# Optimization experiments

Hardware: AMD Instinct MI355X
Metric: run time of the kernel (lower is better)

Reference implementation:

```python
import jax, jax.numpy as jnp
import numpy as np
import math

C = 256
NUM_CLASSES = 80
NUM_CONVS = 4
GROUPS = 32
LEVEL_SHAPES = [(100, 152), (50, 76), (25, 38), (13, 19), (7, 10)]
BATCH = 2


def conv2d(x, w, b):
    # x: [N,C,H,W], w: [O,I,3,3] -> SAME padding, stride 1
    y = jax.lax.conv_general_dilated(x, w, window_strides=(1, 1), padding='SAME',
                                     dimension_numbers=('NCHW', 'OIHW', 'NCHW'))
    return y + b[None, :, None, None]


def group_norm(x, w, b, groups=GROUPS, eps=1e-5):
    N, Ch, H, W = x.shape
    xg = x.reshape(N, groups, Ch // groups, H, W)
    mu = jnp.mean(xg, axis=(2, 3, 4), keepdims=True)
    var = jnp.var(xg, axis=(2, 3, 4), keepdims=True)
    xg = (xg - mu) * jax.lax.rsqrt(var + eps)
    x = xg.reshape(N, Ch, H, W)
    return x * w[None, :, None, None] + b[None, :, None, None]


def tower(x, cw, cb, gw, gb):
    for i in range(NUM_CONVS):
        x = jax.nn.relu(group_norm(conv2d(x, cw[i], cb[i]), gw[i], gb[i]))
    return x


def flatten_head(y, c):
    # [N, A*c, H, W] -> [N, H*W*A, c]  (matches view/permute/reshape in torch)
    N, AC, H, W = y.shape
    A = AC // c
    return y.reshape(N, A, c, H, W).transpose(0, 3, 4, 1, 2).reshape(N, H * W * A, c)


def setup_inputs() -> dict:
    key = jax.random.key(0)
    ks = iter(jax.random.split(key, 64))
    inp = {}
    for i, (h, w) in enumerate(LEVEL_SHAPES):
        inp[f"feat{i}"] = jax.random.normal(next(ks), (BATCH, C, h, w), jnp.float32)
    def cw(shape):  # conv weights init std=0.01 as in torch module
        return jax.random.normal(next(ks), shape, jnp.float32) * 0.01
    inp["cls_conv_w"] = cw((NUM_CONVS, C, C, 3, 3))
    inp["cls_conv_b"] = jnp.zeros((NUM_CONVS, C), jnp.float32)
    inp["cls_gn_w"] = jnp.ones((NUM_CONVS, C), jnp.float32)
    inp["cls_gn_b"] = jnp.zeros((NUM_CONVS, C), jnp.float32)
    inp["cls_out_w"] = cw((NUM_CLASSES, C, 3, 3))
    inp["cls_out_b"] = jnp.full((NUM_CLASSES,), -math.log(99.0), jnp.float32)  # prior prob 0.01
    inp["reg_conv_w"] = cw((NUM_CONVS, C, C, 3, 3))
    inp["reg_conv_b"] = jnp.zeros((NUM_CONVS, C), jnp.float32)
    inp["reg_gn_w"] = jnp.ones((NUM_CONVS, C), jnp.float32)
    inp["reg_gn_b"] = jnp.zeros((NUM_CONVS, C), jnp.float32)
    for name, oc in [("bbox", 4), ("ctr", 1), ("dim", 3), ("ori", 1), ("kp", 16), ("depth", 1)]:
        inp[f"{name}_w"] = cw((oc, C, 3, 3))
        inp[f"{name}_b"] = jnp.zeros((oc,), jnp.float32)
    return inp


def reference(feat0, feat1, feat2, feat3, feat4,
              cls_conv_w, cls_conv_b, cls_gn_w, cls_gn_b, cls_out_w, cls_out_b,
              reg_conv_w, reg_conv_b, reg_gn_w, reg_gn_b,
              bbox_w, bbox_b, ctr_w, ctr_b, dim_w, dim_b,
              ori_w, ori_b, kp_w, kp_b, depth_w, depth_b):
    feats = [feat0, feat1, feat2, feat3, feat4]
    cls_all, bbox_all, ctr_all, dim_all, ori_all, kp_all, depth_all = ([] for _ in range(7))
    for f in feats:
        cf = tower(f, cls_conv_w, cls_conv_b, cls_gn_w, cls_gn_b)
        cls_all.append(flatten_head(conv2d(cf, cls_out_w, cls_out_b), NUM_CLASSES))
        rf = tower(f, reg_conv_w, reg_conv_b, reg_gn_w, reg_gn_b)
        bbox_all.append(flatten_head(jax.nn.relu(conv2d(rf, bbox_w, bbox_b)), 4))
        ctr_all.append(flatten_head(conv2d(rf, ctr_w, ctr_b), 1))
        dim_all.append(flatten_head(conv2d(rf, dim_w, dim_b), 3))
        ori_all.append(flatten_head(conv2d(rf, ori_w, ori_b), 1))
        kp_all.append(flatten_head(conv2d(rf, kp_w, kp_b), 16))
        depth_all.append(flatten_head(conv2d(rf, depth_w, depth_b), 1))
    cat = lambda xs: jnp.concatenate(xs, axis=1)
    return (cat(cls_all), cat(bbox_all), cat(ctr_all), cat(dim_all),
            cat(ori_all), cat(kp_all), cat(depth_all))
```

## Files before the change

kernel.cpp:

```cpp
#include <hip/hip_runtime.h>
#include <stdint.h>

typedef unsigned short ushort_t;
typedef __bf16 bf16x8 __attribute__((ext_vector_type(8)));
typedef float f32x4 __attribute__((ext_vector_type(4)));

#define TOTAL_HW 20267
#define PTOT 21267

__constant__ int d_RB[26] = {3242720,3242720,3242720,3242720, 3404856, 3445390,3445390,3445390,
                             3566992, 3607526,3607526,3607526,3607526,3607526,3607526,3607526,3607526,
                             3607526,3607526,3607526,3607526,3607526,3607526,3607526,3607526, 4256070};
__constant__ int d_RM[26] = {4,4,4,4, 1, 3,3,3, 1, 16,16,16,16,16,16,16,16,16,16,16,16,16,16,16,16, 1};
__constant__ int d_RC[26] = {0,1,2,3, 0, 0,1,2, 0, 0,1,2,3,4,5,6,7,8,9,10,11,12,13,14,15, 0};

__constant__ int F_TC[6]   = {0,238,298,314,318,320};
__constant__ int F_TL[5]   = {119,30,8,2,1};
__constant__ int F_W[5]    = {152,76,38,19,10};
__constant__ int F_HW[5]   = {15200,3800,950,247,70};
__constant__ int F_PB[5]   = {0,15708,19764,20844,21159};
__constant__ int F_LOFF[5] = {0,15200,19000,19950,20197};
__constant__ int F_PC[6]   = {0,508,764,894,962,1000};
__constant__ int F_H[5]    = {100,50,25,13,7};

__device__ __forceinline__ ushort_t f2bf(float f) {
    union { float f; uint32_t i; } x; x.f = f;
    uint32_t r = x.i + 0x7fffu + ((x.i >> 16) & 1u);
    return (ushort_t)(r >> 16);
}
__device__ __forceinline__ float bf2f(ushort_t u) {
    union { uint32_t i; float f; } x; x.i = ((uint32_t)u) << 16; return x.f;
}
__device__ __forceinline__ void gld16(const ushort_t* g, ushort_t* lds) {
    __builtin_amdgcn_global_load_lds((const __attribute__((address_space(1))) void*)g,
                                     (__attribute__((address_space(3))) void*)lds, 16, 0, 0);
}

__global__ __launch_bounds__(256) void wtrans_towerall_k(const float* __restrict__ cw,
                                                         const float* __restrict__ rw,
                                                         ushort_t* __restrict__ dst)
{
    int id = blockIdx.x * 256 + threadIdx.x;
    int g = id >> 16;
    int oc = (id >> 8) & 255, ic = id & 255;
    const float* base = (g >= 4) ? rw : cw;
    int L = g & 3;
    const float* s = base + (size_t)L * 589824 + (size_t)(oc * 256 + ic) * 9;
    ushort_t* d = dst + (size_t)g * 589824 + oc * 256 + ic;
    #pragma unroll
    for (int t = 0; t < 9; t++) d[t * 65536] = f2bf(s[t]);
}
__global__ __launch_bounds__(256) void wtrans_cls_k(const float* __restrict__ src,
                                                    ushort_t* __restrict__ dst)
{
    int id = blockIdx.x * 256 + threadIdx.x;
    int oc = id >> 8, ic = id & 255;
    ushort_t* d = dst + oc * 256 + ic;
    if (oc < 80) {
        const float* s = src + (size_t)(oc * 256 + ic) * 9;
        #pragma unroll
        for (int t = 0; t < 9; t++) d[t * 32768] = f2bf(s[t]);
    } else {
        #pragma unroll
        for (int t = 0; t < 9; t++) d[t * 32768] = 0;
    }
}
__global__ __launch_bounds__(256) void wtrans_reg_k(
    const float* bbox_w, const float* ctr_w, const float* dim_w,
    const float* ori_w,  const float* kp_w,  const float* depth_w,
    const float* bbox_b, const float* ctr_b, const float* dim_b,
    const float* ori_b,  const float* kp_b,  const float* depth_b,
    ushort_t* __restrict__ dst, float* __restrict__ RegBias)
{
    int id = blockIdx.x * 256 + threadIdx.x;
    int oc = id >> 8, ic = id & 255;
    ushort_t* d = dst + oc * 256 + ic;
    if (oc < 26) {
        const float* s; int c;
        if (oc < 4)       { s = bbox_w;  c = oc; }
        else if (oc < 5)  { s = ctr_w;   c = 0; }
        else if (oc < 8)  { s = dim_w;   c = oc - 5; }
        else if (oc < 9)  { s = ori_w;   c = 0; }
        else if (oc < 25) { s = kp_w;    c = oc - 9; }
        else              { s = depth_w; c = 0; }
        const float* sp = s + (size_t)(c * 256 + ic) * 9;
        #pragma unroll
        for (int t = 0; t < 9; t++) d[t * 32768] = f2bf(sp[t]);
    } else {
        #pragma unroll
        for (int t = 0; t < 9; t++) d[t * 32768] = 0;
    }
    if (id < 26) {
        const float* b; int c;
        if (id < 4)       { b = bbox_b;  c = id; }
        else if (id < 5)  { b = ctr_b;   c = 0; }
        else if (id < 8)  { b = dim_b;   c = id - 5; }
        else if (id < 9)  { b = ori_b;   c = 0; }
        else if (id < 25) { b = kp_b;    c = id - 9; }
        else              { b = depth_b; c = 0; }
        RegBias[id] = b[c];
    }
}

__global__ __launch_bounds__(256) void pad_k(ushort_t* b0, ushort_t* b1, ushort_t* b2, ushort_t* b3)
{
    int u = blockIdx.x * 256 + threadIdx.x;
    if (u >= 256000) return;
    int chunk = u & 31; u >>= 5;
    int buf = u & 3; u >>= 2;
    int n = (u >= 1000) ? 1 : 0; int pidx = u - n * 1000;
    int l = 0;
    #pragma unroll
    for (int i = 1; i < 5; i++) if (pidx >= F_PC[i]) l = i;
    int q = pidx - F_PC[l];
    int W = F_W[l], H = F_H[l], Wp = W + 2;
    int py, px;
    if (q < Wp) { py = 0; px = q; }
    else if (q < 2 * Wp) { py = H + 1; px = q - Wp; }
    else { int q2 = q - 2 * Wp; py = 1 + (q2 >> 1); px = (q2 & 1) ? (Wp - 1) : 0; }
    ushort_t* base = b0;
    if (buf == 1) base = b1; else if (buf == 2) base = b2; else if (buf == 3) base = b3;
    *(uint4*)(base + ((size_t)n * PTOT + F_PB[l] + py * Wp + px) * 256 + chunk * 8) = uint4{0u,0u,0u,0u};
}

__global__ __launch_bounds__(256) void packF_k(
    const float* f0, const float* f1, const float* f2,
    const float* f3, const float* f4, ushort_t* __restrict__ S)
{
    __shared__ ushort_t tile[64][65];
    const int PCUM[6] = {0, 1904, 2384, 2504, 2536, 2552};
    const int PT[5]   = {238, 60, 15, 4, 2};
    int bid = blockIdx.x;
    int l = 0;
    #pragma unroll
    for (int i = 1; i < 5; i++) if (bid >= PCUM[i]) l = i;
    int r = bid - PCUM[l];
    int per_n = PT[l] * 4;
    int n = (r >= per_n) ? 1 : 0; r -= n * per_n;
    int pb = r >> 2, cb = r & 3;
    const float* fs = f0;
    if (l == 1) fs = f1; else if (l == 2) fs = f2; else if (l == 3) fs = f3; else if (l == 4) fs = f4;
    int HW = F_HW[l], W = F_W[l], Wp = W + 2;
    int p0 = pb * 64, c0 = cb * 64;
    int t = threadIdx.x;
    #pragma unroll
    for (int i = 0; i < 16; i++) {
        int idx = i * 256 + t; int cl = idx >> 6, pl = idx & 63;
        int p = p0 + pl; ushort_t v = 0;
        if (p < HW) v = f2bf(fs[(size_t)(n * 256 + c0 + cl) * HW + p]);
        tile[cl][pl] = v;
    }
    __syncthreads();
    ushort_t* ob = S + ((size_t)n * PTOT + F_PB[l]) * 256;
    #pragma unroll
    for (int i = 0; i < 16; i++) {
        int idx = i * 256 + t; int pl = idx >> 6, cl = idx & 63;
        int p = p0 + pl;
        if (p < HW) {
            int y = p / W, x = p - y * W;
            ob[((y + 1) * Wp + (x + 1)) * 256 + c0 + cl] = tile[cl][pl];
        }
    }
}

__global__ __launch_bounds__(512, 4) void convT_k(
    const ushort_t* __restrict__ srcC, const ushort_t* __restrict__ srcR,
    ushort_t* __restrict__ dstC, ushort_t* __restrict__ dstR,
    const ushort_t* __restrict__ wtAll,
    const float* __restrict__ biasC, const float* __restrict__ biasR,
    float* __restrict__ stats, int L)
{
    __shared__ __align__(16) ushort_t As[2][8192];
    __shared__ __align__(16) ushort_t Bs[2][8192];

    int gid = blockIdx.x;
    int xcd = gid & 7, idx = gid >> 3;
    int bid = xcd * 40 + (idx >> 2);
    int oc0 = (idx & 1) * 128;
    int tw = (idx >> 1) & 1;

    const ushort_t* src = tw ? srcR : srcC;
    ushort_t* dst = tw ? dstR : dstC;
    const ushort_t* wt = wtAll + (size_t)(tw * 4 + L) * 589824;
    const float* bias = (tw ? biasR : biasC) + L * 256;

    int l = 0;
    #pragma unroll
    for (int i = 1; i < 5; i++) if (bid >= F_TC[i]) l = i;
    int r = bid - F_TC[l];
    int tl = F_TL[l];
    int n = (r >= tl) ? 1 : 0; int tile = r - n * tl;
    int W = F_W[l], HW = F_HW[l], Wp = W + 2;
    int px0 = tile * 128;
    const ushort_t* sbase = src + ((size_t)n * PTOT + F_PB[l]) * 256;
    ushort_t* obase = dst + ((size_t)n * PTOT + F_PB[l]) * 256;

    int tid = threadIdx.x, wv = tid >> 6, ln = tid & 63;
    int wr = wv >> 2, wc = wv & 3;

    int aoff, boff;
    {
        int rloc = wv * 16 + (ln >> 2);
        int p = px0 + rloc; if (p > HW - 1) p = HW - 1;
        int y = p / W, x = p - y * W;
        int c = ((ln & 3) - (rloc >> 1)) & 3;
        aoff = ((y + 1) * Wp + (x + 1)) * 256 + c * 8;
        boff = (oc0 + rloc) * 256 + c * 8;
    }

    auto stage = [&](int it, int b) {
        int tp = it >> 2, q = it & 3;
        int ky = tp / 3, kx = tp - ky * 3;
        int tapo = ((ky - 1) * Wp + (kx - 1)) * 256 + (q << 6);
        const ushort_t* wtap = wt + tp * 65536 + (q << 6);
        gld16(sbase + aoff + tapo,      &As[b][wv * 512]);
        gld16(sbase + aoff + tapo + 32, &As[b][4096 + wv * 512]);
        gld16(wtap + boff,      &Bs[b][wv * 512]);
        gld16(wtap + boff + 32, &Bs[b][4096 + wv * 512]);
    };

    f32x4 acc[4][2];
    #pragma unroll
    for (int mi = 0; mi < 4; mi++)
        #pragma unroll
        for (int ni = 0; ni < 2; ni++) acc[mi][ni] = f32x4{0.f, 0.f, 0.f, 0.f};

    stage(0, 0);

    #pragma unroll 2
    for (int it = 0; it < 36; ++it) {
        asm volatile("s_waitcnt vmcnt(0) lgkmcnt(0)\n\ts_barrier" ::: "memory");
        if (it + 1 < 36) stage(it + 1, (it + 1) & 1);
        int b = it & 1;
        #pragma unroll
        for (int kh = 0; kh < 2; kh++) {
            bf16x8 af[4], bg[2];
            #pragma unroll
            for (int mi = 0; mi < 4; mi++) {
                int rA = wr * 64 + mi * 16 + (ln & 15);
                int ch = ((ln >> 4) + (rA >> 1)) & 3;
                af[mi] = *(const bf16x8*)&As[b][kh * 4096 + rA * 32 + ch * 8];
            }
            #pragma unroll
            for (int ni = 0; ni < 2; ni++) {
                int rB = wc * 32 + ni * 16 + (ln & 15);
                int ch = ((ln >> 4) + (rB >> 1)) & 3;
                bg[ni] = *(const bf16x8*)&Bs[b][kh * 4096 + rB * 32 + ch * 8];
            }
            __builtin_amdgcn_s_setprio(1);
            #pragma unroll
            for (int mi = 0; mi < 4; mi++)
                #pragma unroll
                for (int ni = 0; ni < 2; ni++)
                    acc[mi][ni] = __builtin_amdgcn_mfma_f32_16x16x32_bf16(af[mi], bg[ni], acc[mi][ni], 0, 0, 0);
            __builtin_amdgcn_s_setprio(0);
        }
    }

    #pragma unroll
    for (int ni = 0; ni < 2; ni++) {
        int oc = oc0 + wc * 32 + ni * 16 + (ln & 15);
        float bv = bias[oc];
        float s = 0.f, q = 0.f;
        #pragma unroll
        for (int mi = 0; mi < 4; mi++) {
            int pb = px0 + wr * 64 + mi * 16 + ((ln >> 4) << 2);
            if (pb < HW) {
                int y = pb / W, x = pb - y * W;
                #pragma unroll
                for (int rr2 = 0; rr2 < 4; rr2++) {
                    int p = pb + rr2;
                    if (p < HW) {
                        float v = acc[mi][ni][rr2] + bv;
                        obase[((y + 1) * Wp + (x + 1)) * 256 + oc] = f2bf(v);
                        s += v; q += v * v;
                    }
                    x++; if (x == W) { x = 0; y++; }
                }
            }
        }
        s += __shfl_xor(s, 16, 64); q += __shfl_xor(q, 16, 64);
        s += __shfl_xor(s, 32, 64); q += __shfl_xor(q, 32, 64);
        s += __shfl_xor(s, 1, 64);  q += __shfl_xor(q, 1, 64);
        s += __shfl_xor(s, 2, 64);  q += __shfl_xor(q, 2, 64);
        s += __shfl_xor(s, 4, 64);  q += __shfl_xor(q, 4, 64);
        if (ln == 0 || ln == 8) {
            int g = (oc0 + wc * 32 + ni * 16 + (ln & 8)) >> 3;
            float* st = stats + (size_t)((tw * 4 + L) * 5 + l) * 128 + (n * 32 + g) * 2;
            atomicAdd(st, s); atomicAdd(st + 1, q);
        }
    }
}

__global__ __launch_bounds__(512, 4) void convH_k(
    const ushort_t* __restrict__ srcC, const ushort_t* __restrict__ srcR,
    const ushort_t* __restrict__ wtC, const ushort_t* __restrict__ wtR,
    const float* __restrict__ biasC, const float* __restrict__ biasR,
    float* __restrict__ outF)
{
    __shared__ __align__(16) ushort_t As[2][8192];
    __shared__ __align__(16) ushort_t Bs[2][8192];

    int gid = blockIdx.x;
    int xcd = gid & 7, idx = gid >> 3;
    int bid = xcd * 40 + (idx >> 1);
    int mode = idx & 1;

    const ushort_t* src = mode ? srcR : srcC;
    const ushort_t* wt  = mode ? wtR  : wtC;
    const float* bias   = mode ? biasR : biasC;

    int l = 0;
    #pragma unroll
    for (int i = 1; i < 5; i++) if (bid >= F_TC[i]) l = i;
    int r = bid - F_TC[l];
    int tl = F_TL[l];
    int n = (r >= tl) ? 1 : 0; int tile = r - n * tl;
    int W = F_W[l], HW = F_HW[l], Wp = W + 2;
    int px0 = tile * 128;
    const ushort_t* sbase = src + ((size_t)n * PTOT + F_PB[l]) * 256;

    int tid = threadIdx.x, wv = tid >> 6, ln = tid & 63;
    int wr = wv >> 2, wc = wv & 3;

    int aoff, boff;
    {
        int rloc = wv * 16 + (ln >> 2);
        int p = px0 + rloc; if (p > HW - 1) p = HW - 1;
        int y = p / W, x = p - y * W;
        int c = ((ln & 3) - (rloc >> 1)) & 3;
        aoff = ((y + 1) * Wp + (x + 1)) * 256 + c * 8;
        boff = rloc * 256 + c * 8;
    }

    auto stage = [&](int it, int b) {
        int tp = it >> 2, q = it & 3;
        int ky = tp / 3, kx = tp - ky * 3;
        int tapo = ((ky - 1) * Wp + (kx - 1)) * 256 + (q << 6);
        const ushort_t* wtap = wt + tp * 32768 + (q << 6);
        gld16(sbase + aoff + tapo,      &As[b][wv * 512]);
        gld16(sbase + aoff + tapo + 32, &As[b][4096 + wv * 512]);
        gld16(wtap + boff,      &Bs[b][wv * 512]);
        gld16(wtap + boff + 32, &Bs[b][4096 + wv * 512]);
    };

    f32x4 acc[4][2];
    #pragma unroll
    for (int mi = 0; mi < 4; mi++)
        #pragma unroll
        for (int ni = 0; ni < 2; ni++) acc[mi][ni] = f32x4{0.f, 0.f, 0.f, 0.f};

    stage(0, 0);

    #pragma unroll 2
    for (int it = 0; it < 36; ++it) {
        asm volatile("s_waitcnt vmcnt(0) lgkmcnt(0)\n\ts_barrier" ::: "memory");
        if (it + 1 < 36) stage(it + 1, (it + 1) & 1);
        int b = it & 1;
        #pragma unroll
        for (int kh = 0; kh < 2; kh++) {
            bf16x8 af[4], bg[2];
            #pragma unroll
            for (int mi = 0; mi < 4; mi++) {
                int rA = wr * 64 + mi * 16 + (ln & 15);
                int ch = ((ln >> 4) + (rA >> 1)) & 3;
                af[mi] = *(const bf16x8*)&As[b][kh * 4096 + rA * 32 + ch * 8];
            }
            #pragma unroll
            for (int ni = 0; ni < 2; ni++) {
                int rB = wc * 32 + ni * 16 + (ln & 15);
                int ch = ((ln >> 4) + (rB >> 1)) & 3;
                bg[ni] = *(const bf16x8*)&Bs[b][kh * 4096 + rB * 32 + ch * 8];
            }
            __builtin_amdgcn_s_setprio(1);
            #pragma unroll
            for (int mi = 0; mi < 4; mi++)
                #pragma unroll
                for (int ni = 0; ni < 2; ni++)
                    acc[mi][ni] = __builtin_amdgcn_mfma_f32_16x16x32_bf16(af[mi], bg[ni], acc[mi][ni], 0, 0, 0);
            __builtin_amdgcn_s_setprio(0);
        }
    }

    #pragma unroll
    for (int ni = 0; ni < 2; ni++) {
        int oc = wc * 32 + ni * 16 + (ln & 15);
        bool valid = mode ? (oc < 26) : (oc < 80);
        if (valid) {
            float bv = bias[oc];
            int rb = 0, rm = 80, rc = oc; bool rl = false;
            if (mode) { rb = d_RB[oc]; rm = d_RM[oc]; rc = d_RC[oc]; rl = (oc < 4); }
            #pragma unroll
            for (int mi = 0; mi < 4; mi++) {
                int pb = px0 + wr * 64 + mi * 16 + ((ln >> 4) << 2);
                #pragma unroll
                for (int rr2 = 0; rr2 < 4; rr2++) {
                    int p = pb + rr2;
                    if (p < HW) {
                        float v = acc[mi][ni][rr2] + bv;
                        if (rl) v = fmaxf(v, 0.f);
                        int pg = n * TOTAL_HW + F_LOFF[l] + p;
                        outF[rb + (size_t)pg * rm + rc] = v;
                    }
                }
            }
        }
    }
}

__global__ __launch_bounds__(256) void normF_k(
    ushort_t* __restrict__ bufC, ushort_t* __restrict__ bufR,
    const float* __restrict__ stats,
    const float* __restrict__ gwC, const float* __restrict__ gwR,
    const float* __restrict__ gbC, const float* __restrict__ gbR, int L)
{
    int u = blockIdx.x * 256 + threadIdx.x;
    if (u >= 2594176) return;
    int tw = (u >= 1297088) ? 1 : 0; u -= tw * 1297088;
    int n = (u >= 648544) ? 1 : 0; u -= n * 648544;
    int cp = u >> 5, g = u & 31;
    int l = 0;
    #pragma unroll
    for (int i = 1; i < 5; i++) if (cp >= F_LOFF[i]) l = i;
    int p = cp - F_LOFF[l];
    int W = F_W[l], HW = F_HW[l];
    int y = p / W, x = p - y * W;
    const float* st = stats + (size_t)((tw * 4 + L) * 5 + l) * 128 + (n * 32 + g) * 2;
    float cnt = 8.0f * (float)HW;
    float mean = st[0] / cnt;
    float var = st[1] / cnt - mean * mean;
    float inv = rsqrtf(fmaxf(var, 0.f) + 1e-5f);
    const float* gw = (tw ? gwR : gwC) + L * 256 + g * 8;
    const float* gb = (tw ? gbR : gbC) + L * 256 + g * 8;
    ushort_t* buf = tw ? bufR : bufC;
    ushort_t* ptr = buf + (((size_t)n * PTOT + F_PB[l]) + (y + 1) * (W + 2) + (x + 1)) * 256 + g * 8;
    uint4 din = *(const uint4*)ptr;
    uint4 dout;
    const ushort_t* xi = (const ushort_t*)&din;
    ushort_t* oi = (ushort_t*)&dout;
    #pragma unroll
    for (int i = 0; i < 8; i++) {
        float v = (bf2f(xi[i]) - mean) * inv * gw[i] + gb[i];
        oi[i] = f2bf(fmaxf(v, 0.f));
    }
    *(uint4*)ptr = dout;
}


extern "C" void kernel_launch(void* const* d_in, const int* in_sizes, int n_in,
                              void* d_out, int out_size, void* d_ws, size_t ws_size,
                              hipStream_t stream) {
    const float* feats[5] = {(const float*)d_in[0], (const float*)d_in[1],
                             (const float*)d_in[2], (const float*)d_in[3],
                             (const float*)d_in[4]};
    const float* cls_conv_w = (const float*)d_in[5];
    const float* cls_conv_b = (const float*)d_in[6];
    const float* cls_gn_w   = (const float*)d_in[7];
    const float* cls_gn_b   = (const float*)d_in[8];
    const float* cls_out_w  = (const float*)d_in[9];
    const float* cls_out_b  = (const float*)d_in[10];
    const float* reg_conv_w = (const float*)d_in[11];
    const float* reg_conv_b = (const float*)d_in[12];
    const float* reg_gn_w   = (const float*)d_in[13];
    const float* reg_gn_b   = (const float*)d_in[14];

    char* wsb = (char*)d_ws;
    float* Stats     = (float*)wsb;
    float* RegBias   = (float*)(wsb + 20480);
    ushort_t* TowerWtAll = (ushort_t*)(wsb + 20608);
    ushort_t* WtCls  = (ushort_t*)(wsb + 9457792);
    ushort_t* WtReg  = (ushort_t*)(wsb + 10047616);
    ushort_t* S  = (ushort_t*)(wsb + 10637440);
    ushort_t* Ac = (ushort_t*)(wsb + 32414848);
    ushort_t* Ar = (ushort_t*)(wsb + 54192256);
    ushort_t* Br = (ushort_t*)(wsb + 75969664);
    float* outf  = (float*)d_out;

    hipMemsetAsync(d_ws, 0, 20608, stream);
    pad_k<<<1000, 256, 0, stream>>>(S, Ac, Ar, Br);

    wtrans_towerall_k<<<2048, 256, 0, stream>>>(cls_conv_w, reg_conv_w, TowerWtAll);
    wtrans_cls_k<<<128, 256, 0, stream>>>(cls_out_w, WtCls);
    wtrans_reg_k<<<128, 256, 0, stream>>>(
        (const float*)d_in[15], (const float*)d_in[17], (const float*)d_in[19],
        (const float*)d_in[21], (const float*)d_in[23], (const float*)d_in[25],
        (const float*)d_in[16], (const float*)d_in[18], (const float*)d_in[20],
        (const float*)d_in[22], (const float*)d_in[24], (const float*)d_in[26],
        WtReg, RegBias);

    packF_k<<<2552, 256, 0, stream>>>(feats[0], feats[1], feats[2], feats[3], feats[4], S);

    ushort_t* sc[4] = {S,  Ac, S,  Ac};
    ushort_t* dc[4] = {Ac, S,  Ac, S };
    ushort_t* sr[4] = {S,  Ar, Br, Ar};
    ushort_t* dr[4] = {Ar, Br, Ar, Br};
    for (int L = 0; L < 4; L++) {
        convT_k<<<1280, 512, 0, stream>>>(
            sc[L], sr[L], dc[L], dr[L], TowerWtAll, cls_conv_b, reg_conv_b, Stats, L);
        normF_k<<<10134, 256, 0, stream>>>(
            dc[L], dr[L], Stats, cls_gn_w, reg_gn_w, cls_gn_b, reg_gn_b, L);
    }
    convH_k<<<640, 512, 0, stream>>>(S, Br, WtCls, WtReg, cls_out_b, RegBias, outf);
}
```

Baseline: 789.9 us.

## Split K across wave halves with 64x64 warp tiles and LDS reduction

Both conv kernels change the wave layout from 2x4 waves each doing both K-halves of a 128x128 tile to a 2x2 spatial grid with two K-split groups. Each wave now computes a 64x64 sub-tile over one K-half, doubling MFMA work per LDS fragment load and cutting LDS read traffic per MFMA. The partial sums are then exchanged through shared memory and reduced, with each wave of a pair finishing half of the output columns. This doubles the accumulator registers and adds an epilogue LDS round trip plus two barriers, which may hurt occupancy under the 512x4 launch bounds.

```diff
diff --git a/kernel.cpp b/kernel.cpp
--- a/kernel.cpp
+++ b/kernel.cpp
@@ -170,8 +170,7 @@
     const float* __restrict__ biasC, const float* __restrict__ biasR,
     float* __restrict__ stats, int L)
 {
-    __shared__ __align__(16) ushort_t As[2][8192];
-    __shared__ __align__(16) ushort_t Bs[2][8192];
+    __shared__ __align__(16) ushort_t SH[32768];
 
     int gid = blockIdx.x;
     int xcd = gid & 7, idx = gid >> 3;
@@ -196,7 +195,7 @@
     ushort_t* obase = dst + ((size_t)n * PTOT + F_PB[l]) * 256;
 
     int tid = threadIdx.x, wv = tid >> 6, ln = tid & 63;
-    int wr = wv >> 2, wc = wv & 3;
+    int wr = (wv >> 1) & 1, wc = wv & 1, kh = wv >> 2;
 
     int aoff, boff;
     {
@@ -213,17 +212,17 @@
         int ky = tp / 3, kx = tp - ky * 3;
         int tapo = ((ky - 1) * Wp + (kx - 1)) * 256 + (q << 6);
         const ushort_t* wtap = wt + tp * 65536 + (q << 6);
-        gld16(sbase + aoff + tapo,      &As[b][wv * 512]);
-        gld16(sbase + aoff + tapo + 32, &As[b][4096 + wv * 512]);
-        gld16(wtap + boff,      &Bs[b][wv * 512]);
-        gld16(wtap + boff + 32, &Bs[b][4096 + wv * 512]);
+        gld16(sbase + aoff + tapo,      &SH[b * 8192 + wv * 512]);
+        gld16(sbase + aoff + tapo + 32, &SH[b * 8192 + 4096 + wv * 512]);
+        gld16(wtap + boff,      &SH[16384 + b * 8192 + wv * 512]);
+        gld16(wtap + boff + 32, &SH[16384 + b * 8192 + 4096 + wv * 512]);
     };
 
-    f32x4 acc[4][2];
+    f32x4 acc[4][4];
     #pragma unroll
     for (int mi = 0; mi < 4; mi++)
         #pragma unroll
-        for (int ni = 0; ni < 2; ni++) acc[mi][ni] = f32x4{0.f, 0.f, 0.f, 0.f};
+        for (int ni = 0; ni < 4; ni++) acc[mi][ni] = f32x4{0.f, 0.f, 0.f, 0.f};
 
     stage(0, 0);
 
@@ -232,34 +231,49 @@
         asm volatile("s_waitcnt vmcnt(0) lgkmcnt(0)\n\ts_barrier" ::: "memory");
         if (it + 1 < 36) stage(it + 1, (it + 1) & 1);
         int b = it & 1;
-        #pragma unroll
-        for (int kh = 0; kh < 2; kh++) {
-            bf16x8 af[4], bg[2];
+        bf16x8 af[4], bg[4];
+        #pragma unroll
+        for (int mi = 0; mi < 4; mi++) {
+            int rA = wr * 64 + mi * 16 + (ln & 15);
+            int ch = ((ln >> 4) + (rA >> 1)) & 3;
+            af[mi] = *(const bf16x8*)&SH[b * 8192 + kh * 4096 + rA * 32 + ch * 8];
+        }
+        #pragma unroll
+        for (int ni = 0; ni < 4; ni++) {
+            int rB = wc * 64 + ni * 16 + (ln & 15);
+            int ch = ((ln >> 4) + (rB >> 1)) & 3;
+            bg[ni] = *(const bf16x8*)&SH[16384 + b * 8192 + kh * 4096 + rB * 32 + ch * 8];
+        }
+        __builtin_amdgcn_s_setprio(1);
+        #pragma unroll
+        for (int mi = 0; mi < 4; mi++)
             #pragma unroll
-            for (int mi = 0; mi < 4; mi++) {
-                int rA = wr * 64 + mi * 16 + (ln & 15);
-                int ch = ((ln >> 4) + (rA >> 1)) & 3;
-                af[mi] = *(const bf16x8*)&As[b][kh * 4096 + rA * 32 + ch * 8];
-            }
-            #pragma unroll
-            for (int ni = 0; ni < 2; ni++) {
-                int rB = wc * 32 + ni * 16 + (ln & 15);
-                int ch = ((ln >> 4) + (rB >> 1)) & 3;
-                bg[ni] = *(const bf16x8*)&Bs[b][kh * 4096 + rB * 32 + ch * 8];
-            }
-            __builtin_amdgcn_s_setprio(1);
-            #pragma unroll
-            for (int mi = 0; mi < 4; mi++)
-                #pragma unroll
-                for (int ni = 0; ni < 2; ni++)
-                    acc[mi][ni] = __builtin_amdgcn_mfma_f32_16x16x32_bf16(af[mi], bg[ni], acc[mi][ni], 0, 0, 0);
-            __builtin_amdgcn_s_setprio(0);
-        }
-    }
-
-    #pragma unroll
-    for (int ni = 0; ni < 2; ni++) {
-        int oc = oc0 + wc * 32 + ni * 16 + (ln & 15);
+            for (int ni = 0; ni < 4; ni++)
+                acc[mi][ni] = __builtin_amdgcn_mfma_f32_16x16x32_bf16(af[mi], bg[ni], acc[mi][ni], 0, 0, 0);
+        __builtin_amdgcn_s_setprio(0);
+    }
+
+    __syncthreads();
+    f32x4* F4 = (f32x4*)SH;
+    int prt = wv ^ 4;
+    int wbase = kh ? 0 : 2;
+    int rbase = kh ? 2 : 0;
+    #pragma unroll
+    for (int mi = 0; mi < 4; mi++)
+        #pragma unroll
+        for (int h = 0; h < 2; h++)
+            F4[wv * 512 + ln * 8 + ((mi * 2 + h) ^ (ln & 7))] = acc[mi][wbase + h];
+    __syncthreads();
+    #pragma unroll
+    for (int mi = 0; mi < 4; mi++)
+        #pragma unroll
+        for (int h = 0; h < 2; h++)
+            acc[mi][rbase + h] += F4[prt * 512 + ln * 8 + ((mi * 2 + h) ^ (ln & 7))];
+
+    #pragma unroll
+    for (int h = 0; h < 2; h++) {
+        int ni = rbase + h;
+        int oc = oc0 + wc * 64 + ni * 16 + (ln & 15);
         float bv = bias[oc];
         float s = 0.f, q = 0.f;
         #pragma unroll
@@ -285,7 +299,7 @@
         s += __shfl_xor(s, 2, 64);  q += __shfl_xor(q, 2, 64);
         s += __shfl_xor(s, 4, 64);  q += __shfl_xor(q, 4, 64);
         if (ln == 0 || ln == 8) {
-            int g = (oc0 + wc * 32 + ni * 16 + (ln & 8)) >> 3;
+            int g = (oc0 + wc * 64 + ni * 16 + (ln & 8)) >> 3;
             float* st = stats + (size_t)((tw * 4 + L) * 5 + l) * 128 + (n * 32 + g) * 2;
             atomicAdd(st, s); atomicAdd(st + 1, q);
         }
@@ -298,8 +312,7 @@
     const float* __restrict__ biasC, const float* __restrict__ biasR,
     float* __restrict__ outF)
 {
-    __shared__ __align__(16) ushort_t As[2][8192];
-    __shared__ __align__(16) ushort_t Bs[2][8192];
+    __shared__ __align__(16) ushort_t SH[32768];
 
     int gid = blockIdx.x;
     int xcd = gid & 7, idx = gid >> 3;
@@ -321,7 +334,7 @@
     const ushort_t* sbase = src + ((size_t)n * PTOT + F_PB[l]) * 256;
 
     int tid = threadIdx.x, wv = tid >> 6, ln = tid & 63;
-    int wr = wv >> 2, wc = wv & 3;
+    int wr = (wv >> 1) & 1, wc = wv & 1, kh = wv >> 2;
 
     int aoff, boff;
     {
@@ -338,17 +351,17 @@
         int ky = tp / 3, kx = tp - ky * 3;
         int tapo = ((ky - 1) * Wp + (kx - 1)) * 256 + (q << 6);
         const ushort_t* wtap = wt + tp * 32768 + (q << 6);
-        gld16(sbase + aoff + tapo,      &As[b][wv * 512]);
-        gld16(sbase + aoff + tapo + 32, &As[b][4096 + wv * 512]);
-        gld16(wtap + boff,      &Bs[b][wv * 512]);
-        gld16(wtap + boff + 32, &Bs[b][4096 + wv * 512]);
+        gld16(sbase + aoff + tapo,      &SH[b * 8192 + wv * 512]);
+        gld16(sbase + aoff + tapo + 32, &SH[b * 8192 + 4096 + wv * 512]);
+        gld16(wtap + boff,      &SH[16384 + b * 8192 + wv * 512]);
+        gld16(wtap + boff + 32, &SH[16384 + b * 8192 + 4096 + wv * 512]);
     };
 
-    f32x4 acc[4][2];
+    f32x4 acc[4][4];
     #pragma unroll
     for (int mi = 0; mi < 4; mi++)
         #pragma unroll
-        for (int ni = 0; ni < 2; ni++) acc[mi][ni] = f32x4{0.f, 0.f, 0.f, 0.f};
+        for (int ni = 0; ni < 4; ni++) acc[mi][ni] = f32x4{0.f, 0.f, 0.f, 0.f};
 
     stage(0, 0);
 
@@ -357,34 +370,49 @@
         asm volatile("s_waitcnt vmcnt(0) lgkmcnt(0)\n\ts_barrier" ::: "memory");
         if (it + 1 < 36) stage(it + 1, (it + 1) & 1);
         int b = it & 1;
-        #pragma unroll
-        for (int kh = 0; kh < 2; kh++) {
-            bf16x8 af[4], bg[2];
+        bf16x8 af[4], bg[4];
+        #pragma unroll
+        for (int mi = 0; mi < 4; mi++) {
+            int rA = wr * 64 + mi * 16 + (ln & 15);
+            int ch = ((ln >> 4) + (rA >> 1)) & 3;
+            af[mi] = *(const bf16x8*)&SH[b * 8192 + kh * 4096 + rA * 32 + ch * 8];
+        }
+        #pragma unroll
+        for (int ni = 0; ni < 4; ni++) {
+            int rB = wc * 64 + ni * 16 + (ln & 15);
+            int ch = ((ln >> 4) + (rB >> 1)) & 3;
+            bg[ni] = *(const bf16x8*)&SH[16384 + b * 8192 + kh * 4096 + rB * 32 + ch * 8];
+        }
+        __builtin_amdgcn_s_setprio(1);
+        #pragma unroll
+        for (int mi = 0; mi < 4; mi++)
             #pragma unroll
-            for (int mi = 0; mi < 4; mi++) {
-                int rA = wr * 64 + mi * 16 + (ln & 15);
-                int ch = ((ln >> 4) + (rA >> 1)) & 3;
-                af[mi] = *(const bf16x8*)&As[b][kh * 4096 + rA * 32 + ch * 8];
-            }
-            #pragma unroll
-            for (int ni = 0; ni < 2; ni++) {
-                int rB = wc * 32 + ni * 16 + (ln & 15);
-                int ch = ((ln >> 4) + (rB >> 1)) & 3;
-                bg[ni] = *(const bf16x8*)&Bs[b][kh * 4096 + rB * 32 + ch * 8];
-            }
-            __builtin_amdgcn_s_setprio(1);
-            #pragma unroll
-            for (int mi = 0; mi < 4; mi++)
-                #pragma unroll
-                for (int ni = 0; ni < 2; ni++)
-                    acc[mi][ni] = __builtin_amdgcn_mfma_f32_16x16x32_bf16(af[mi], bg[ni], acc[mi][ni], 0, 0, 0);
-            __builtin_amdgcn_s_setprio(0);
-        }
-    }
-
-    #pragma unroll
-    for (int ni = 0; ni < 2; ni++) {
-        int oc = wc * 32 + ni * 16 + (ln & 15);
+            for (int ni = 0; ni < 4; ni++)
+                acc[mi][ni] = __builtin_amdgcn_mfma_f32_16x16x32_bf16(af[mi], bg[ni], acc[mi][ni], 0, 0, 0);
+        __builtin_amdgcn_s_setprio(0);
+    }
+
+    __syncthreads();
+    f32x4* F4 = (f32x4*)SH;
+    int prt = wv ^ 4;
+    int wbase = kh ? 0 : 2;
+    int rbase = kh ? 2 : 0;
+    #pragma unroll
+    for (int mi = 0; mi < 4; mi++)
+        #pragma unroll
+        for (int h = 0; h < 2; h++)
+            F4[wv * 512 + ln * 8 + ((mi * 2 + h) ^ (ln & 7))] = acc[mi][wbase + h];
+    __syncthreads();
+    #pragma unroll
+    for (int mi = 0; mi < 4; mi++)
+        #pragma unroll
+        for (int h = 0; h < 2; h++)
+            acc[mi][rbase + h] += F4[prt * 512 + ln * 8 + ((mi * 2 + h) ^ (ln & 7))];
+
+    #pragma unroll
+    for (int h = 0; h < 2; h++) {
+        int ni = rbase + h;
+        int oc = wc * 64 + ni * 16 + (ln & 15);
         bool valid = mode ? (oc < 26) : (oc < 80);
         if (valid) {
             float bv = bias[oc];
```

Result: slower. 1.108 ms (+40.3%).
